# Performance work log

Measured on AMD Instinct MI355X. Metric: run time of the kernel, lower is better.

Reference implementation:

```python
import jax, jax.numpy as jnp
import numpy as np

NEG_SLOPE = 0.2  # self.alpha


def setup_inputs() -> dict:
    key = jax.random.key(0)
    k1, k2, k3, k4 = jax.random.split(key, 4)
    N, E, in_dim, out_dim = 50000, 800000, 128, 64
    inp = jax.random.normal(k1, (N, in_dim), dtype=jnp.float32)
    edge = jax.random.randint(k2, (2, E), 0, N, dtype=jnp.int64)
    # xavier_normal init scales
    W = jax.random.normal(k3, (in_dim, out_dim), dtype=jnp.float32) * np.sqrt(2.0 / (in_dim + out_dim))
    a = jax.random.normal(k4, (2 * out_dim, 1), dtype=jnp.float32) * np.sqrt(2.0 / (2 * out_dim + 1))
    return {"input": inp, "edge": edge, "W": W, "a": a}


def reference(input, edge, W, a):
    # eval mode: dropout is a no-op
    N = input.shape[0]
    h = input @ W                           # [N, out_dim]
    src, dst = edge[0], edge[1]             # [E], [E]
    out_dim = h.shape[1]
    a_src, a_dst = a[:out_dim, 0], a[out_dim:, 0]
    # equivalent to cat([h[src], h[dst]], 1) @ a, without materializing [E, 2*out_dim]
    score = (h @ a_src)[src] + (h @ a_dst)[dst]          # [E]
    e = jax.nn.leaky_relu(score, negative_slope=NEG_SLOPE)
    # sparse softmax over each row (segment by src)
    m = jax.ops.segment_max(e, src, num_segments=N)      # [N], -inf for empty rows
    m = jnp.where(jnp.isfinite(m), m, 0.0)
    ex = jnp.exp(e - m[src])                             # [E]
    s = jax.ops.segment_sum(ex, src, num_segments=N)     # [N]
    attn = ex / s[src]                                   # [E]
    # scatter-aggregate: out[i] = sum_{(i,j) in E} attn_ij * h[j]
    out = jax.ops.segment_sum(attn[:, None] * h[dst], src, num_segments=N)  # [N, out_dim]
    return jax.nn.elu(out)
```

## Files before the change

kernel.cpp:

```cpp
#include <hip/hip_runtime.h>
#include <hip/hip_fp16.h>
#include <math.h>

#define IN_DIM 128
#define OUT_DIM 64
#define NEG_SLOPE 0.2f

#define BUCKET_SRCS 32
#define CAP 1024
#define MAXBK 2048

typedef _Float16 half8 __attribute__((ext_vector_type(8)));
typedef float floatx4 __attribute__((ext_vector_type(4)));

#define GR 64
#define PA_CHUNK 8192

__global__ __launch_bounds__(256) void fused_gp(
    const float* __restrict__ in, const float* __restrict__ W,
    const float* __restrict__ a, __half* __restrict__ hb,
    float* __restrict__ hs, float* __restrict__ hd,
    const int* __restrict__ src, const int* __restrict__ dst,
    int* __restrict__ gcursor, int* __restrict__ pairbuf,
    int E, int NBK, int PB, int N)
{
    __shared__ union {
        struct { _Float16 Al[GR][IN_DIM]; _Float16 Wt[OUT_DIM][IN_DIM + 8]; } g;
        struct { int lcount[MAXBK]; int lbase[MAXBK]; int lrun[MAXBK]; } p;
    } sm;

    const int t = threadIdx.x;

    if ((int)blockIdx.x < PB) {
        for (int i = t; i < NBK; i += 256) sm.p.lcount[i] = 0;
        __syncthreads();

        const int base = blockIdx.x * PA_CHUNK;
        int w[32];
        int nev = 0;
        #pragma unroll
        for (int j = 0; j < 8; ++j) {
            int i = base + j * 1024 + t * 4;
            if (i + 3 < E) {
                int4 s4 = *(const int4*)&src[i];
                int4 d4 = *(const int4*)&dst[i];
                int b0 = s4.x >> 5, b1 = s4.y >> 5, b2 = s4.z >> 5, b3 = s4.w >> 5;
                w[4 * j + 0] = (b0 << 21) | ((s4.x & 31) << 16) | d4.x;
                w[4 * j + 1] = (b1 << 21) | ((s4.y & 31) << 16) | d4.y;
                w[4 * j + 2] = (b2 << 21) | ((s4.z & 31) << 16) | d4.z;
                w[4 * j + 3] = (b3 << 21) | ((s4.w & 31) << 16) | d4.w;
                atomicAdd(&sm.p.lcount[b0], 1);
                atomicAdd(&sm.p.lcount[b1], 1);
                atomicAdd(&sm.p.lcount[b2], 1);
                atomicAdd(&sm.p.lcount[b3], 1);
                nev = 4 * j + 4;
            } else {
                #pragma unroll
                for (int u = 0; u < 4; ++u) {
                    if (i + u < E) {
                        int s = src[i + u];
                        int d = dst[i + u];
                        int bb = s >> 5;
                        w[4 * j + u] = (bb << 21) | ((s & 31) << 16) | d;
                        atomicAdd(&sm.p.lcount[bb], 1);
                        nev = 4 * j + u + 1;
                    }
                }
            }
        }
        __syncthreads();
        for (int i = t; i < NBK; i += 256) {
            int c = sm.p.lcount[i];
            int gb = 0;
            if (c > 0) gb = atomicAdd(&gcursor[i], c);
            sm.p.lbase[i] = i * CAP + gb;
            sm.p.lrun[i] = 0;
        }
        __syncthreads();
        #pragma unroll
        for (int k = 0; k < 32; ++k) {
            if (k < nev) {
                int bb = ((unsigned)w[k]) >> 21;
                int r = atomicAdd(&sm.p.lrun[bb], 1);
                int pos = sm.p.lbase[bb] + r;
                if (pos - bb * CAP < CAP)
                    pairbuf[pos] = w[k];
            }
        }
        return;
    }

    const int r0 = (blockIdx.x - PB) * GR;

    #pragma unroll
    for (int i = 0; i < 8; ++i) {
        int q = i * 256 + t;
        int row = q >> 5;
        int kq  = (q & 31) * 4;
        int grow = r0 + row; if (grow >= N) grow = N - 1;
        float4 v = *(const float4*)&in[(size_t)grow * IN_DIM + kq];
        union { __half2 h2[2]; uint2 u; } cv;
        cv.h2[0] = __floats2half2_rn(v.x, v.y);
        cv.h2[1] = __floats2half2_rn(v.z, v.w);
        *(uint2*)&sm.g.Al[row][kq] = cv.u;
    }
    #pragma unroll
    for (int i = 0; i < 8; ++i) {
        int q = i * 256 + t;
        int k  = q >> 4;
        int n4 = (q & 15) * 4;
        float4 v = *(const float4*)&W[(size_t)k * OUT_DIM + n4];
        sm.g.Wt[n4 + 0][k] = (_Float16)v.x;
        sm.g.Wt[n4 + 1][k] = (_Float16)v.y;
        sm.g.Wt[n4 + 2][k] = (_Float16)v.z;
        sm.g.Wt[n4 + 3][k] = (_Float16)v.w;
    }
    __syncthreads();

    const int lane = t & 63;
    const int wave = t >> 6;
    const int m16  = lane & 15;
    const int quad = lane >> 4;

    floatx4 acc[4];
    #pragma unroll
    for (int nt = 0; nt < 4; ++nt) acc[nt] = (floatx4){0.f, 0.f, 0.f, 0.f};

    #pragma unroll
    for (int kc = 0; kc < 4; ++kc) {
        half8 af = *(const half8*)&sm.g.Al[wave * 16 + m16][kc * 32 + quad * 8];
        #pragma unroll
        for (int nt = 0; nt < 4; ++nt) {
            half8 bf = *(const half8*)&sm.g.Wt[nt * 16 + m16][kc * 32 + quad * 8];
            acc[nt] = __builtin_amdgcn_mfma_f32_16x16x32_f16(af, bf, acc[nt], 0, 0, 0);
        }
    }
    __syncthreads();

    _Float16 (*Crep)[OUT_DIM + 8] = (_Float16(*)[OUT_DIM + 8])&sm.g.Al[0][0];

    float asl[4], adl[4];
    #pragma unroll
    for (int nt = 0; nt < 4; ++nt) {
        asl[nt] = a[nt * 16 + m16];
        adl[nt] = a[OUT_DIM + nt * 16 + m16];
    }
    #pragma unroll
    for (int r = 0; r < 4; ++r) {
        float ps = 0.f, pd = 0.f;
        #pragma unroll
        for (int nt = 0; nt < 4; ++nt) {
            ps = fmaf(acc[nt][r], asl[nt], ps);
            pd = fmaf(acc[nt][r], adl[nt], pd);
        }
        #pragma unroll
        for (int off = 1; off < 16; off <<= 1) {
            ps += __shfl_xor(ps, off, 64);
            pd += __shfl_xor(pd, off, 64);
        }
        if (m16 == 0) {
            int row = r0 + wave * 16 + quad * 4 + r;
            if (row < N) { hs[row] = ps; hd[row] = pd; }
        }
    }

    #pragma unroll
    for (int nt = 0; nt < 4; ++nt)
        #pragma unroll
        for (int r = 0; r < 4; ++r)
            Crep[wave * 16 + quad * 4 + r][nt * 16 + m16] = (_Float16)acc[nt][r];
    __syncthreads();
    #pragma unroll
    for (int i = 0; i < 2; ++i) {
        int idx = i * 256 + t;
        int row = idx >> 3;
        int seg = idx & 7;
        int gr2 = r0 + row;
        if (gr2 < N) {
            uint4 v = *(const uint4*)&Crep[row][seg * 8];
            *(uint4*)&hb[(size_t)gr2 * OUT_DIM + seg * 8] = v;
        }
    }
}

__global__ __launch_bounds__(256) void node_kernel(
    const __half* __restrict__ hb, const float* __restrict__ hs,
    const float* __restrict__ hd, const int* __restrict__ gcursor,
    const int* __restrict__ pairbuf, float* __restrict__ out, int N)
{
    __shared__ int2  spair[CAP];
    __shared__ float hsl[BUCKET_SRCS];
    __shared__ int   cnt[BUCKET_SRCS];
    __shared__ int   excl[BUCKET_SRCS];
    __shared__ int   lcur[BUCKET_SRCS];
    __shared__ int   perm[BUCKET_SRCS];

    const int t = threadIdx.x;
    const int b = blockIdx.x;
    const int M = min(gcursor[b], CAP);

    if (t < BUCKET_SRCS) {
        int node = b * BUCKET_SRCS + t;
        hsl[t] = (node < N) ? hs[node] : 0.f;
        cnt[t] = 0;
    }
    __syncthreads();

    const int i0 = t * 4;
    int4 p4 = *(const int4*)&pairbuf[b * CAP + i0];
    int   pkv[4] = {p4.x, p4.y, p4.z, p4.w};
    int   dofs[4], slv[4];
    float exv[4];
    int nl = 0;
    #pragma unroll
    for (int u = 0; u < 4; ++u) {
        if (i0 + u < M) {
            int pk = pkv[u];
            int sl = (pk >> 16) & 31;
            int d  = pk & 0xffff;
            float e = hsl[sl] + hd[d];
            e = (e >= 0.f) ? e : NEG_SLOPE * e;
            exv[u]  = __expf(e);
            slv[u]  = sl;
            dofs[u] = d << 7;
            atomicAdd(&cnt[sl], 1);
            nl = u + 1;
        }
    }
    __syncthreads();
    if (t < BUCKET_SRCS) {
        int raw = cnt[t];
        int v = raw;
        #pragma unroll
        for (int off = 1; off < BUCKET_SRCS; off <<= 1) {
            int u = __shfl_up(v, off, 64);
            if (t >= off) v += u;
        }
        excl[t] = v - raw;
        lcur[t] = v - raw;

        int key = raw * 32 + t;
        #pragma unroll
        for (int k = 2; k <= 32; k <<= 1) {
            #pragma unroll
            for (int j = k >> 1; j > 0; j >>= 1) {
                int other = __shfl_xor(key, j, 64);
                bool up = (t & k) == 0;
                bool lower = (t & j) == 0;
                int mn = min(key, other), mx = max(key, other);
                key = (up == lower) ? mn : mx;
            }
        }
        perm[t] = key & 31;
    }
    __syncthreads();
    #pragma unroll
    for (int u = 0; u < 4; ++u) {
        if (u < nl) {
            int r = atomicAdd(&lcur[slv[u]], 1);
            spair[r] = make_int2(__float_as_int(exv[u]), dofs[u]);
        }
    }
    __syncthreads();

    const int lane = t & 63;
    const int wave = t >> 6;
    const int slot = lane >> 3;
    const int c8   = lane & 7;
    const int loc  = perm[wave * 8 + slot];
    const int node = b * BUCKET_SRCS + loc;
    const bool valid = node < N;

    const int deg = cnt[loc];
    const int beg = excl[loc];

    int dmax = deg;
    #pragma unroll
    for (int off = 8; off < 64; off <<= 1)
        dmax = max(dmax, __shfl_xor(dmax, off, 64));

    const char* hbp = (const char*)hb + c8 * 16;

    float acc[8];
    float ssum = 0.f;
    #pragma unroll
    for (int q = 0; q < 8; ++q) acc[q] = 0.f;

    for (int j = 0; j < dmax; j += 4) {
        int2 pr[4];
        float ex[4];
        #pragma unroll
        for (int u = 0; u < 4; ++u) {
            bool act = j + u < deg;
            pr[u] = spair[beg + (act ? j + u : 0)];
            ex[u] = act ? __int_as_float(pr[u].x) : 0.f;
            ssum += ex[u];
        }
        union { uint4 u4; __half2 h2[4]; } hv[4];
        #pragma unroll
        for (int u = 0; u < 4; ++u)
            hv[u].u4 = *(const uint4*)(hbp + pr[u].y);
        #pragma unroll
        for (int u = 0; u < 4; ++u)
            #pragma unroll
            for (int q = 0; q < 4; ++q) {
                acc[2 * q]     = fmaf(ex[u], __low2float(hv[u].h2[q]),  acc[2 * q]);
                acc[2 * q + 1] = fmaf(ex[u], __high2float(hv[u].h2[q]), acc[2 * q + 1]);
            }
    }

    if (valid) {
        float inv = (deg > 0) ? 1.f / ssum : 0.f;
        float o[8];
        #pragma unroll
        for (int q = 0; q < 8; ++q) {
            float v = acc[q] * inv;
            o[q] = (v > 0.f) ? v : (__expf(v) - 1.f);
        }
        float4 o0 = {o[0], o[1], o[2], o[3]};
        float4 o1 = {o[4], o[5], o[6], o[7]};
        *(float4*)&out[(size_t)node * OUT_DIM + c8 * 8] = o0;
        *(float4*)&out[(size_t)node * OUT_DIM + c8 * 8 + 4] = o1;
    }
}

extern "C" void kernel_launch(void* const* d_in, const int* in_sizes, int n_in,
                              void* d_out, int out_size, void* d_ws, size_t ws_size,
                              hipStream_t stream)
{
    const float* input = (const float*)d_in[0];
    const int*   edge  = (const int*)d_in[1];
    const float* W     = (const float*)d_in[2];
    const float* a     = (const float*)d_in[3];
    float* out = (float*)d_out;

    const int N = in_sizes[0] / IN_DIM;
    const int E = in_sizes[1] / 2;
    const int* src = edge;
    const int* dst = edge + E;

    const int NBK = (N + BUCKET_SRCS - 1) / BUCKET_SRCS;
    const int PB  = (E + PA_CHUNK - 1) / PA_CHUNK;
    const int GB  = (N + GR - 1) / GR;

    size_t idx = 0;
    int* gcursor = (int*)d_ws + idx; idx += MAXBK;
    int* pairbuf = (int*)d_ws + idx; idx += (size_t)NBK * CAP;
    __half* hb = (__half*)((int*)d_ws + idx); idx += (size_t)N * OUT_DIM / 2;
    float* hs = (float*)((int*)d_ws + idx); idx += N;
    float* hd = (float*)((int*)d_ws + idx); idx += N;

    hipMemsetAsync(gcursor, 0, MAXBK * sizeof(int), stream);
    fused_gp<<<PB + GB, 256, 0, stream>>>(
        input, W, a, hb, hs, hd, src, dst, gcursor, pairbuf, E, NBK, PB, N);
    node_kernel<<<NBK, 256, 0, stream>>>(hb, hs, hd, gcursor, pairbuf, out, N);
}
```

Measured before the change: 114.4 us.

## Merge GEMM, bucketing and aggregation into one persistent cooperative kernel

Replaces the memset plus two kernel launches with a single cooperative kernel of up to 1024 persistent blocks. Blocks pull work items from atomic queues, first running the projection GEMM and the edge bucketing, then a grid-wide sync, then the per-bucket softmax aggregation. This is meant to remove launch gaps, the separate memset and tail imbalance between stages. In exchange it pays grid-barrier cost and fixes occupancy at two blocks per CU. The old two-kernel path remains as a fallback if the cooperative launch fails.

```diff
diff --git a/kernel.cpp b/kernel.cpp
--- a/kernel.cpp
+++ b/kernel.cpp
@@ -1,6 +1,9 @@
 #include <hip/hip_runtime.h>
 #include <hip/hip_fp16.h>
+#include <hip/hip_cooperative_groups.h>
 #include <math.h>
+
+namespace cg = cooperative_groups;
 
 #define IN_DIM 128
 #define OUT_DIM 64
@@ -15,6 +18,333 @@
 
 #define GR 64
 #define PA_CHUNK 8192
+
+__global__ __launch_bounds__(256, 2) void gat_all(
+    const float* __restrict__ in, const float* __restrict__ W,
+    const float* __restrict__ a, __half* __restrict__ hb,
+    float* __restrict__ hs, float* __restrict__ hd,
+    const int* __restrict__ src, const int* __restrict__ dst,
+    int* __restrict__ gcursor, int* __restrict__ pairbuf,
+    float* __restrict__ out,
+    int E, int NBK, int PB, int NITEM, int N)
+{
+    __shared__ union {
+        struct { _Float16 Al[GR][IN_DIM]; _Float16 Wt[OUT_DIM][IN_DIM + 8]; } g;
+        struct { int lcount[MAXBK]; int lbase[MAXBK]; int lrun[MAXBK]; } p;
+        struct { int2 spair[CAP]; float hsl[BUCKET_SRCS];
+                 int cnt[BUCKET_SRCS]; int excl[BUCKET_SRCS];
+                 int lcur[BUCKET_SRCS]; int perm[BUCKET_SRCS]; } n;
+    } sm;
+    __shared__ int s_item;
+
+    const int t = threadIdx.x;
+    cg::grid_group grid = cg::this_grid();
+
+    for (int i = blockIdx.x * 256 + t; i < MAXBK; i += gridDim.x * 256)
+        gcursor[i] = 0;
+
+    __threadfence();
+    grid.sync();
+
+    int* wqA = &gcursor[MAXBK - 2];
+    int* wqB = &gcursor[MAXBK - 1];
+
+    for (;;) {
+        __syncthreads();
+        if (t == 0) s_item = atomicAdd(wqA, 1);
+        __syncthreads();
+        const int item = s_item;
+        if (item >= NITEM) break;
+
+        if (item < PB) {
+            for (int i = t; i < NBK; i += 256) sm.p.lcount[i] = 0;
+            __syncthreads();
+
+            const int base = item * PA_CHUNK;
+            int w[32];
+            int nev = 0;
+            #pragma unroll
+            for (int j = 0; j < 8; ++j) {
+                int i = base + j * 1024 + t * 4;
+                if (i + 3 < E) {
+                    int4 s4 = *(const int4*)&src[i];
+                    int4 d4 = *(const int4*)&dst[i];
+                    int b0 = s4.x >> 5, b1 = s4.y >> 5, b2 = s4.z >> 5, b3 = s4.w >> 5;
+                    w[4 * j + 0] = (b0 << 21) | ((s4.x & 31) << 16) | d4.x;
+                    w[4 * j + 1] = (b1 << 21) | ((s4.y & 31) << 16) | d4.y;
+                    w[4 * j + 2] = (b2 << 21) | ((s4.z & 31) << 16) | d4.z;
+                    w[4 * j + 3] = (b3 << 21) | ((s4.w & 31) << 16) | d4.w;
+                    atomicAdd(&sm.p.lcount[b0], 1);
+                    atomicAdd(&sm.p.lcount[b1], 1);
+                    atomicAdd(&sm.p.lcount[b2], 1);
+                    atomicAdd(&sm.p.lcount[b3], 1);
+                    nev = 4 * j + 4;
+                } else {
+                    #pragma unroll
+                    for (int u = 0; u < 4; ++u) {
+                        if (i + u < E) {
+                            int s = src[i + u];
+                            int d = dst[i + u];
+                            int bb = s >> 5;
+                            w[4 * j + u] = (bb << 21) | ((s & 31) << 16) | d;
+                            atomicAdd(&sm.p.lcount[bb], 1);
+                            nev = 4 * j + u + 1;
+                        }
+                    }
+                }
+            }
+            __syncthreads();
+            for (int i = t; i < NBK; i += 256) {
+                int c = sm.p.lcount[i];
+                int gb = 0;
+                if (c > 0) gb = atomicAdd(&gcursor[i], c);
+                sm.p.lbase[i] = i * CAP + gb;
+                sm.p.lrun[i] = 0;
+            }
+            __syncthreads();
+            #pragma unroll
+            for (int k = 0; k < 32; ++k) {
+                if (k < nev) {
+                    int bb = ((unsigned)w[k]) >> 21;
+                    int r = atomicAdd(&sm.p.lrun[bb], 1);
+                    int pos = sm.p.lbase[bb] + r;
+                    if (pos - bb * CAP < CAP)
+                        pairbuf[pos] = w[k];
+                }
+            }
+        } else {
+            const int r0 = (item - PB) * GR;
+
+            #pragma unroll
+            for (int i = 0; i < 8; ++i) {
+                int q = i * 256 + t;
+                int row = q >> 5;
+                int kq  = (q & 31) * 4;
+                int grow = r0 + row; if (grow >= N) grow = N - 1;
+                float4 v = *(const float4*)&in[(size_t)grow * IN_DIM + kq];
+                union { __half2 h2[2]; uint2 u; } cv;
+                cv.h2[0] = __floats2half2_rn(v.x, v.y);
+                cv.h2[1] = __floats2half2_rn(v.z, v.w);
+                *(uint2*)&sm.g.Al[row][kq] = cv.u;
+            }
+            #pragma unroll
+            for (int i = 0; i < 8; ++i) {
+                int q = i * 256 + t;
+                int k  = q >> 4;
+                int n4 = (q & 15) * 4;
+                float4 v = *(const float4*)&W[(size_t)k * OUT_DIM + n4];
+                sm.g.Wt[n4 + 0][k] = (_Float16)v.x;
+                sm.g.Wt[n4 + 1][k] = (_Float16)v.y;
+                sm.g.Wt[n4 + 2][k] = (_Float16)v.z;
+                sm.g.Wt[n4 + 3][k] = (_Float16)v.w;
+            }
+            __syncthreads();
+
+            const int lane = t & 63;
+            const int wave = t >> 6;
+            const int m16  = lane & 15;
+            const int quad = lane >> 4;
+
+            floatx4 acc[4];
+            #pragma unroll
+            for (int nt = 0; nt < 4; ++nt) acc[nt] = (floatx4){0.f, 0.f, 0.f, 0.f};
+
+            #pragma unroll
+            for (int kc = 0; kc < 4; ++kc) {
+                half8 af = *(const half8*)&sm.g.Al[wave * 16 + m16][kc * 32 + quad * 8];
+                #pragma unroll
+                for (int nt = 0; nt < 4; ++nt) {
+                    half8 bf = *(const half8*)&sm.g.Wt[nt * 16 + m16][kc * 32 + quad * 8];
+                    acc[nt] = __builtin_amdgcn_mfma_f32_16x16x32_f16(af, bf, acc[nt], 0, 0, 0);
+                }
+            }
+            __syncthreads();
+
+            _Float16 (*Crep)[OUT_DIM + 8] = (_Float16(*)[OUT_DIM + 8])&sm.g.Al[0][0];
+
+            float asl[4], adl[4];
+            #pragma unroll
+            for (int nt = 0; nt < 4; ++nt) {
+                asl[nt] = a[nt * 16 + m16];
+                adl[nt] = a[OUT_DIM + nt * 16 + m16];
+            }
+            #pragma unroll
+            for (int r = 0; r < 4; ++r) {
+                float ps = 0.f, pd = 0.f;
+                #pragma unroll
+                for (int nt = 0; nt < 4; ++nt) {
+                    ps = fmaf(acc[nt][r], asl[nt], ps);
+                    pd = fmaf(acc[nt][r], adl[nt], pd);
+                }
+                #pragma unroll
+                for (int off = 1; off < 16; off <<= 1) {
+                    ps += __shfl_xor(ps, off, 64);
+                    pd += __shfl_xor(pd, off, 64);
+                }
+                if (m16 == 0) {
+                    int row = r0 + wave * 16 + quad * 4 + r;
+                    if (row < N) { hs[row] = ps; hd[row] = pd; }
+                }
+            }
+
+            #pragma unroll
+            for (int nt = 0; nt < 4; ++nt)
+                #pragma unroll
+                for (int r = 0; r < 4; ++r)
+                    Crep[wave * 16 + quad * 4 + r][nt * 16 + m16] = (_Float16)acc[nt][r];
+            __syncthreads();
+            #pragma unroll
+            for (int i = 0; i < 2; ++i) {
+                int idx = i * 256 + t;
+                int row = idx >> 3;
+                int seg = idx & 7;
+                int gr2 = r0 + row;
+                if (gr2 < N) {
+                    uint4 v = *(const uint4*)&Crep[row][seg * 8];
+                    *(uint4*)&hb[(size_t)gr2 * OUT_DIM + seg * 8] = v;
+                }
+            }
+        }
+    }
+
+    __threadfence();
+    grid.sync();
+    __threadfence();
+
+    for (;;) {
+        __syncthreads();
+        if (t == 0) s_item = atomicAdd(wqB, 1);
+        __syncthreads();
+        const int b = s_item;
+        if (b >= NBK) break;
+
+        const int M = min(gcursor[b], CAP);
+
+        if (t < BUCKET_SRCS) {
+            int node = b * BUCKET_SRCS + t;
+            sm.n.hsl[t] = (node < N) ? hs[node] : 0.f;
+            sm.n.cnt[t] = 0;
+        }
+        __syncthreads();
+
+        const int i0 = t * 4;
+        int4 p4 = *(const int4*)&pairbuf[b * CAP + i0];
+        int   pkv[4] = {p4.x, p4.y, p4.z, p4.w};
+        int   dofs[4], slv[4];
+        float exv[4];
+        int nl = 0;
+        #pragma unroll
+        for (int u = 0; u < 4; ++u) {
+            if (i0 + u < M) {
+                int pk = pkv[u];
+                int sl = (pk >> 16) & 31;
+                int d  = pk & 0xffff;
+                float e = sm.n.hsl[sl] + hd[d];
+                e = (e >= 0.f) ? e : NEG_SLOPE * e;
+                exv[u]  = __expf(e);
+                slv[u]  = sl;
+                dofs[u] = d << 7;
+                atomicAdd(&sm.n.cnt[sl], 1);
+                nl = u + 1;
+            }
+        }
+        __syncthreads();
+        if (t < BUCKET_SRCS) {
+            int raw = sm.n.cnt[t];
+            int v = raw;
+            #pragma unroll
+            for (int off = 1; off < BUCKET_SRCS; off <<= 1) {
+                int u = __shfl_up(v, off, 64);
+                if (t >= off) v += u;
+            }
+            sm.n.excl[t] = v - raw;
+            sm.n.lcur[t] = v - raw;
+
+            int key = raw * 32 + t;
+            #pragma unroll
+            for (int k = 2; k <= 32; k <<= 1) {
+                #pragma unroll
+                for (int j = k >> 1; j > 0; j >>= 1) {
+                    int other = __shfl_xor(key, j, 64);
+                    bool up = (t & k) == 0;
+                    bool lower = (t & j) == 0;
+                    int mn = min(key, other), mx = max(key, other);
+                    key = (up == lower) ? mn : mx;
+                }
+            }
+            sm.n.perm[t] = key & 31;
+        }
+        __syncthreads();
+        #pragma unroll
+        for (int u = 0; u < 4; ++u) {
+            if (u < nl) {
+                int r = atomicAdd(&sm.n.lcur[slv[u]], 1);
+                sm.n.spair[r] = make_int2(__float_as_int(exv[u]), dofs[u]);
+            }
+        }
+        __syncthreads();
+
+        const int lane = t & 63;
+        const int wave = t >> 6;
+        const int slot = lane >> 3;
+        const int c8   = lane & 7;
+        const int loc  = sm.n.perm[wave * 8 + slot];
+        const int node = b * BUCKET_SRCS + loc;
+        const bool valid = node < N;
+
+        const int deg = sm.n.cnt[loc];
+        const int beg = sm.n.excl[loc];
+
+        int dmax = deg;
+        #pragma unroll
+        for (int off = 8; off < 64; off <<= 1)
+            dmax = max(dmax, __shfl_xor(dmax, off, 64));
+
+        const char* hbp = (const char*)hb + c8 * 16;
+
+        float acc[8];
+        float ssum = 0.f;
+        #pragma unroll
+        for (int q = 0; q < 8; ++q) acc[q] = 0.f;
+
+        for (int j = 0; j < dmax; j += 4) {
+            int2 pr[4];
+            float ex[4];
+            #pragma unroll
+            for (int u = 0; u < 4; ++u) {
+                bool act = j + u < deg;
+                pr[u] = sm.n.spair[beg + (act ? j + u : 0)];
+                ex[u] = act ? __int_as_float(pr[u].x) : 0.f;
+                ssum += ex[u];
+            }
+            union { uint4 u4; __half2 h2[4]; } hv[4];
+            #pragma unroll
+            for (int u = 0; u < 4; ++u)
+                hv[u].u4 = *(const uint4*)(hbp + pr[u].y);
+            #pragma unroll
+            for (int u = 0; u < 4; ++u)
+                #pragma unroll
+                for (int q = 0; q < 4; ++q) {
+                    acc[2 * q]     = fmaf(ex[u], __low2float(hv[u].h2[q]),  acc[2 * q]);
+                    acc[2 * q + 1] = fmaf(ex[u], __high2float(hv[u].h2[q]), acc[2 * q + 1]);
+                }
+        }
+
+        if (valid) {
+            float inv = (deg > 0) ? 1.f / ssum : 0.f;
+            float o[8];
+            #pragma unroll
+            for (int q = 0; q < 8; ++q) {
+                float v = acc[q] * inv;
+                o[q] = (v > 0.f) ? v : (__expf(v) - 1.f);
+            }
+            float4 o0 = {o[0], o[1], o[2], o[3]};
+            float4 o1 = {o[4], o[5], o[6], o[7]};
+            *(float4*)&out[(size_t)node * OUT_DIM + c8 * 8] = o0;
+            *(float4*)&out[(size_t)node * OUT_DIM + c8 * 8 + 4] = o1;
+        }
+    }
+}
 
 __global__ __launch_bounds__(256) void fused_gp(
     const float* __restrict__ in, const float* __restrict__ W,
@@ -336,12 +666,13 @@
 
     const int N = in_sizes[0] / IN_DIM;
     const int E = in_sizes[1] / 2;
-    const int* src = edge;
-    const int* dst = edge + E;
+    const int* srcp = edge;
+    const int* dstp = edge + E;
 
     const int NBK = (N + BUCKET_SRCS - 1) / BUCKET_SRCS;
     const int PB  = (E + PA_CHUNK - 1) / PA_CHUNK;
     const int GB  = (N + GR - 1) / GR;
+    int NITEM = PB + GB;
 
     size_t idx = 0;
     int* gcursor = (int*)d_ws + idx; idx += MAXBK;
@@ -350,8 +681,39 @@
     float* hs = (float*)((int*)d_ws + idx); idx += N;
     float* hd = (float*)((int*)d_ws + idx); idx += N;
 
-    hipMemsetAsync(gcursor, 0, MAXBK * sizeof(int), stream);
-    fused_gp<<<PB + GB, 256, 0, stream>>>(
-        input, W, a, hb, hs, hd, src, dst, gcursor, pairbuf, E, NBK, PB, N);
-    node_kernel<<<NBK, 256, 0, stream>>>(hb, hs, hd, gcursor, pairbuf, out, N);
+    static int coop_blocks = -1;
+    if (coop_blocks < 0) {
+        int bpc = 0;
+        hipError_t e = hipOccupancyMaxActiveBlocksPerMultiprocessor(
+            &bpc, gat_all, 256, 0);
+        if (e == hipSuccess && bpc >= 1) {
+            coop_blocks = bpc * 256;
+            if (coop_blocks > 1024) coop_blocks = 1024;
+        } else {
+            coop_blocks = 0;
+        }
+    }
+
+    bool done = false;
+    if (coop_blocks >= 256) {
+        void* args[] = { (void*)&input, (void*)&W, (void*)&a, (void*)&hb,
+                         (void*)&hs, (void*)&hd, (void*)&srcp, (void*)&dstp,
+                         (void*)&gcursor, (void*)&pairbuf, (void*)&out,
+                         (void*)&E, (void*)&NBK, (void*)&PB, (void*)&NITEM,
+                         (void*)&N };
+        hipError_t e = hipLaunchCooperativeKernel(
+            (const void*)gat_all, dim3(coop_blocks), dim3(256), args, 0, stream);
+        if (e == hipSuccess) {
+            done = true;
+        } else {
+            coop_blocks = 0;
+        }
+    }
+
+    if (!done) {
+        hipMemsetAsync(gcursor, 0, MAXBK * sizeof(int), stream);
+        fused_gp<<<PB + GB, 256, 0, stream>>>(
+            input, W, a, hb, hs, hd, srcp, dstp, gcursor, pairbuf, E, NBK, PB, N);
+        node_kernel<<<NBK, 256, 0, stream>>>(hb, hs, hd, gcursor, pairbuf, out, N);
+    }
 }
```

After: 254.1 us. 2.22x slower.
